# Performance work log

Hardware: AMD Instinct MI355X
Metric: run time of the kernel (lower is better)

Reference implementation:

```python
import jax, jax.numpy as jnp
import numpy as np

N, D_IN, D_K = 8192, 512, 64


def setup_inputs() -> dict:
    key = jax.random.key(0)
    k0, k1, k2, k3 = jax.random.split(key, 4)
    return {
        "inputs": jax.random.normal(k0, (N, D_IN), dtype=jnp.float32),
        "Wq": jax.random.normal(k1, (D_K, D_IN), dtype=jnp.float32),
        "Wk": jax.random.normal(k2, (D_K, D_IN), dtype=jnp.float32),
        "Wv": jax.random.normal(k3, (D_K, D_IN), dtype=jnp.float32),
    }


def reference(inputs, Wq, Wk, Wv):
    # nn.Linear(bias=False): x @ W.T, W has shape [out, in]
    q = inputs @ Wq.T  # [N, Dk]
    k = inputs @ Wk.T  # [N, Dk]
    v = inputs @ Wv.T  # [N, Dk]
    scaled = (q @ k.T) / jnp.sqrt(jnp.float32(D_K))  # [N, N]
    attn = jax.nn.softmax(scaled, axis=1)            # softmax over keys (dim=1)
    # weighted = values[:,None] * attn.T[:,:,None]; sum over dim 0 == attn @ v
    return attn @ v  # [N, Dk]
```

## Files before the change

kernel.cpp:

```cpp
#include <hip/hip_runtime.h>
#include <hip/hip_bf16.h>


#define N_TOK 8192
#define D_INN 512
#define DK    64

typedef __attribute__((ext_vector_type(8))) short bf16x8;
typedef __attribute__((ext_vector_type(4))) float f32x4;

static __device__ __forceinline__ unsigned f2bf_u(float f) {
  union { float f; unsigned u; } v; v.f = f;
  return (v.u + 0x7FFFu + ((v.u >> 16) & 1u)) >> 16;
}
static __device__ __forceinline__ unsigned short f2bf(float f) { return (unsigned short)f2bf_u(f); }
static __device__ __forceinline__ float bf2f(unsigned short h) {
  union { unsigned u; float f; } v; v.u = ((unsigned)h) << 16; return v.f;
}
static __device__ __forceinline__ unsigned truncpk(float a, float b) {
  union { float f; unsigned u; } x, y; x.f = a; y.f = b;
  return (x.u >> 16) | (y.u & 0xFFFF0000u);
}
static __device__ __forceinline__ void split2(float a, float b, unsigned& hi, unsigned& lo) {
  unsigned ha = f2bf_u(a), hb = f2bf_u(b);
  float ra = a - bf2f((unsigned short)ha);
  float rb = b - bf2f((unsigned short)hb);
  hi = ha | (hb << 16);
  lo = f2bf_u(ra) | (f2bf_u(rb) << 16);
}
static __device__ __forceinline__ void split8(const float* p, bf16x8& hi, bf16x8& lo) {
  float4 a = *(const float4*)p;
  float4 b = *(const float4*)(p + 4);
  union { unsigned u[4]; bf16x8 v; } H, L;
  split2(a.x, a.y, H.u[0], L.u[0]);
  split2(a.z, a.w, H.u[1], L.u[1]);
  split2(b.x, b.y, H.u[2], L.u[2]);
  split2(b.z, b.w, H.u[3], L.u[3]);
  hi = H.v; lo = L.v;
}
static __device__ __forceinline__ bf16x8 round8(const float* p) {
  float4 a = *(const float4*)p;
  float4 b = *(const float4*)(p + 4);
  union { unsigned u[4]; bf16x8 v; } H;
  H.u[0] = f2bf_u(a.x) | (f2bf_u(a.y) << 16);
  H.u[1] = f2bf_u(a.z) | (f2bf_u(a.w) << 16);
  H.u[2] = f2bf_u(b.x) | (f2bf_u(b.y) << 16);
  H.u[3] = f2bf_u(b.z) | (f2bf_u(b.w) << 16);
  return H.v;
}

__global__ __launch_bounds__(256, 2) void qkv3(
    const float* __restrict__ X,
    const float* __restrict__ Wq, const float* __restrict__ Wk, const float* __restrict__ Wv,
    unsigned short* __restrict__ qhp, unsigned short* __restrict__ qlp,
    unsigned short* __restrict__ kph, unsigned short* __restrict__ kpl,
    unsigned short* __restrict__ vp) {
  const int tid = threadIdx.x, w = tid >> 6, l = tid & 63;
  const int l15 = l & 15, g = l >> 4;
  const int t0 = blockIdx.x * 16;
  const int dq = w * 16;

  f32x4 aq = {0.f, 0.f, 0.f, 0.f}, ak = aq, av = aq;

  for (int kc = 0; kc < D_INN; kc += 32) {
    bf16x8 ah, al;
    split8(X + (t0 + l15) * D_INN + kc + g * 8, ah, al);

    const int woff = (dq + l15) * D_INN + kc + g * 8;
    bf16x8 bqh, bql, bkh, bkl;
    split8(Wq + woff, bqh, bql);
    split8(Wk + woff, bkh, bkl);
    bf16x8 bvh = round8(Wv + woff);

    aq = __builtin_amdgcn_mfma_f32_16x16x32_bf16(ah, bqh, aq, 0, 0, 0);
    aq = __builtin_amdgcn_mfma_f32_16x16x32_bf16(ah, bql, aq, 0, 0, 0);
    aq = __builtin_amdgcn_mfma_f32_16x16x32_bf16(al, bqh, aq, 0, 0, 0);
    ak = __builtin_amdgcn_mfma_f32_16x16x32_bf16(ah, bkh, ak, 0, 0, 0);
    ak = __builtin_amdgcn_mfma_f32_16x16x32_bf16(ah, bkl, ak, 0, 0, 0);
    ak = __builtin_amdgcn_mfma_f32_16x16x32_bf16(al, bkh, ak, 0, 0, 0);
    av = __builtin_amdgcn_mfma_f32_16x16x32_bf16(ah, bvh, av, 0, 0, 0);
    av = __builtin_amdgcn_mfma_f32_16x16x32_bf16(al, bvh, av, 0, 0, 0);
  }

#pragma unroll
  for (int r = 0; r < 4; r++) {
    float v = aq[r] * 0.125f;
    int row = t0 + g * 4 + r;
    unsigned short h = f2bf(v);
    qhp[row * DK + dq + l15] = h;
    qlp[row * DK + dq + l15] = f2bf(v - bf2f(h));
  }
#pragma unroll
  for (int r = 0; r < 4; r++) {
    float v = ak[r];
    int t = t0 + g * 4 + r;
    int d = dq + l15;
    int off = (t >> 5) * 2048 + ((t >> 4) & 1) * 1024 + (d >> 5) * 512 +
              ((t & 15) + (((d >> 3) & 3) << 4)) * 8 + (d & 7);
    unsigned short h = f2bf(v);
    kph[off] = h;
    kpl[off] = f2bf(v - bf2f(h));
  }
  {
    int tg = t0 + g * 4;
    int d = dq + l15;
    int off = (tg >> 5) * 2048 + (d >> 4) * 512 +
              (((d & 15) + (((tg >> 3) & 3) << 4))) * 8 + (tg & 7);
    uint2 pk;
    pk.x = f2bf_u(av[0]) | (f2bf_u(av[1]) << 16);
    pk.y = f2bf_u(av[2]) | (f2bf_u(av[3]) << 16);
    *(uint2*)(vp + off) = pk;
  }
}

__global__ __launch_bounds__(256, 2) void attn4(
    const unsigned short* __restrict__ qhp, const unsigned short* __restrict__ qlp,
    const unsigned short* __restrict__ kph, const unsigned short* __restrict__ kpl,
    const unsigned short* __restrict__ vp,
    unsigned short* __restrict__ pnb, float* __restrict__ pden, float* __restrict__ pM) {
  __shared__ unsigned short P_lds[4 * 2 * 16 * 72];

  const int tid = threadIdx.x, w = tid >> 6, l = tid & 63;
  const int l15 = l & 15, g = l >> 4;
  const int qblk = blockIdx.x >> 4, ks = blockIdx.x & 15;
  const int wq0 = qblk * 128 + w * 32;

  bf16x8 qhf[2][2], qlf[2][2];
#pragma unroll
  for (int u = 0; u < 2; u++)
#pragma unroll
    for (int c = 0; c < 2; c++) {
      int row = wq0 + u * 16 + l15;
      qhf[u][c] = *(const bf16x8*)(qhp + row * DK + c * 32 + g * 8);
      qlf[u][c] = *(const bf16x8*)(qlp + row * DK + c * 32 + g * 8);
    }

  const short onec = (short)0x3F80;
  const bf16x8 ones = {onec, onec, onec, onec, onec, onec, onec, onec};

  f32x4 accO[2][4], accL[2];
  float m[2] = {-1e30f, -1e30f};
#pragma unroll
  for (int u = 0; u < 2; u++) {
    accL[u] = f32x4{0.f, 0.f, 0.f, 0.f};
#pragma unroll
    for (int ds = 0; ds < 4; ds++) accO[u][ds] = f32x4{0.f, 0.f, 0.f, 0.f};
  }

  for (int kt = ks * 512; kt < ks * 512 + 512; kt += 64) {
    const int kti = kt >> 5;

    f32x4 st[2][4];
#pragma unroll
    for (int s = 0; s < 4; s++) {
      bf16x8 khf[2], klf[2];
#pragma unroll
      for (int c = 0; c < 2; c++) {
        const int off = (kti + (s >> 1)) * 2048 + (s & 1) * 1024 + c * 512 + l * 8;
        khf[c] = *(const bf16x8*)(kph + off);
        klf[c] = *(const bf16x8*)(kpl + off);
      }
      __builtin_amdgcn_s_setprio(1);
#pragma unroll
      for (int u = 0; u < 2; u++) {
        f32x4 sa = {0.f, 0.f, 0.f, 0.f};
        sa = __builtin_amdgcn_mfma_f32_16x16x32_bf16(khf[0], qhf[u][0], sa, 0, 0, 0);
        sa = __builtin_amdgcn_mfma_f32_16x16x32_bf16(khf[1], qhf[u][1], sa, 0, 0, 0);
        sa = __builtin_amdgcn_mfma_f32_16x16x32_bf16(khf[0], qlf[u][0], sa, 0, 0, 0);
        sa = __builtin_amdgcn_mfma_f32_16x16x32_bf16(khf[1], qlf[u][1], sa, 0, 0, 0);
        sa = __builtin_amdgcn_mfma_f32_16x16x32_bf16(klf[0], qhf[u][0], sa, 0, 0, 0);
        sa = __builtin_amdgcn_mfma_f32_16x16x32_bf16(klf[1], qhf[u][1], sa, 0, 0, 0);
        st[u][s] = sa;
      }
      __builtin_amdgcn_s_setprio(0);
    }

    bf16x8 vb[4][2];
#pragma unroll
    for (int ds = 0; ds < 4; ds++)
#pragma unroll
      for (int c = 0; c < 2; c++)
        vb[ds][c] = *(const bf16x8*)(vp + (kti + c) * 2048 + ds * 512 + l * 8);

    bf16x8 pa[2][2];
#pragma unroll
    for (int u = 0; u < 2; u++) {
      float t0m = fmaxf(fmaxf(st[u][0][0], st[u][0][1]), fmaxf(st[u][0][2], st[u][0][3]));
      float t1m = fmaxf(fmaxf(st[u][1][0], st[u][1][1]), fmaxf(st[u][1][2], st[u][1][3]));
      float t2m = fmaxf(fmaxf(st[u][2][0], st[u][2][1]), fmaxf(st[u][2][2], st[u][2][3]));
      float t3m = fmaxf(fmaxf(st[u][3][0], st[u][3][1]), fmaxf(st[u][3][2], st[u][3][3]));
      float tm = fmaxf(fmaxf(t0m, t1m), fmaxf(t2m, t3m));
      tm = fmaxf(tm, __shfl_xor(tm, 16, 64));
      tm = fmaxf(tm, __shfl_xor(tm, 32, 64));
      if (__any(tm > m[u] + 8.f)) {
        float mn = fmaxf(m[u], tm);
        float fac = __expf(m[u] - mn);
        m[u] = mn;
#pragma unroll
        for (int r = 0; r < 4; r++) {
          float fr = __shfl(fac, g * 4 + r, 64);
          accL[u][r] *= fr;
#pragma unroll
          for (int ds = 0; ds < 4; ds++) accO[u][ds][r] *= fr;
        }
      }
      const int base = ((w * 2 + u) * 16 + l15) * 72;
#pragma unroll
      for (int s = 0; s < 4; s++) {
        float p0 = __expf(st[u][s][0] - m[u]);
        float p1 = __expf(st[u][s][1] - m[u]);
        float p2 = __expf(st[u][s][2] - m[u]);
        float p3 = __expf(st[u][s][3] - m[u]);
        *(unsigned*)&P_lds[base + s * 16 + g * 4]     = truncpk(p0, p1);
        *(unsigned*)&P_lds[base + s * 16 + g * 4 + 2] = truncpk(p2, p3);
      }
#pragma unroll
      for (int c = 0; c < 2; c++)
        pa[u][c] = *(const bf16x8*)&P_lds[base + c * 32 + g * 8];
      accL[u] = __builtin_amdgcn_mfma_f32_16x16x32_bf16(pa[u][0], ones, accL[u], 0, 0, 0);
      accL[u] = __builtin_amdgcn_mfma_f32_16x16x32_bf16(pa[u][1], ones, accL[u], 0, 0, 0);
    }

    __builtin_amdgcn_s_setprio(1);
#pragma unroll
    for (int ds = 0; ds < 4; ds++)
#pragma unroll
      for (int u = 0; u < 2; u++) {
        accO[u][ds] = __builtin_amdgcn_mfma_f32_16x16x32_bf16(pa[u][0], vb[ds][0], accO[u][ds], 0, 0, 0);
        accO[u][ds] = __builtin_amdgcn_mfma_f32_16x16x32_bf16(pa[u][1], vb[ds][1], accO[u][ds], 0, 0, 0);
      }
    __builtin_amdgcn_s_setprio(0);
  }

#pragma unroll
  for (int u = 0; u < 2; u++) {
#pragma unroll
    for (int ds = 0; ds < 4; ds++)
#pragma unroll
      for (int r = 0; r < 4; r++)
        pnb[(size_t)ks * (N_TOK * DK) + (wq0 + u * 16 + g * 4 + r) * DK + ds * 16 + l15] =
            f2bf(accO[u][ds][r]);
    if (l15 == 0) {
#pragma unroll
      for (int r = 0; r < 4; r++) pden[ks * N_TOK + wq0 + u * 16 + g * 4 + r] = accL[u][r];
    }
    if (g == 0) pM[ks * N_TOK + wq0 + u * 16 + l15] = m[u];
  }
}

__global__ __launch_bounds__(256) void merge16(
    const unsigned short* __restrict__ pnb, const float* __restrict__ pden,
    const float* __restrict__ pM, float* __restrict__ out) {
  int i = blockIdx.x * 256 + threadIdx.x;
  int q = i >> 6, d = i & 63;
  float M = -1e30f;
#pragma unroll
  for (int s = 0; s < 16; s++) M = fmaxf(M, pM[s * N_TOK + q]);
  float num = 0.f, den = 0.f;
#pragma unroll
  for (int s = 0; s < 16; s++) {
    float e = __expf(pM[s * N_TOK + q] - M);
    num += bf2f(pnb[(size_t)s * (N_TOK * DK) + q * DK + d]) * e;
    den += pden[s * N_TOK + q] * e;
  }
  out[i] = num / den;
}

extern "C" void kernel_launch(void* const* d_in, const int* in_sizes, int n_in,
                              void* d_out, int out_size, void* d_ws, size_t ws_size,
                              hipStream_t stream) {
  (void)in_sizes; (void)n_in; (void)out_size; (void)ws_size;
  const float* X  = (const float*)d_in[0];
  const float* Wq = (const float*)d_in[1];
  const float* Wk = (const float*)d_in[2];
  const float* Wv = (const float*)d_in[3];

  char* base = (char*)d_ws;
  unsigned short* pnb = (unsigned short*)(base);
  unsigned short* qhp = (unsigned short*)(base + 16777216);
  unsigned short* qlp = (unsigned short*)(base + 17825792);
  unsigned short* kph = (unsigned short*)(base + 18874368);
  unsigned short* kpl = (unsigned short*)(base + 19922944);
  unsigned short* vp  = (unsigned short*)(base + 20971520);
  float* pden = (float*)(base + 22020096);
  float* pM   = (float*)(base + 22544384);

  qkv3<<<N_TOK / 16, 256, 0, stream>>>(X, Wq, Wk, Wv, qhp, qlp, kph, kpl, vp);
  attn4<<<1024, 256, 0, stream>>>(qhp, qlp, kph, kpl, vp, pnb, pden, pM);
  merge16<<<(N_TOK * DK) / 256, 256, 0, stream>>>(pnb, pden, pM, (float*)d_out);
}
```

Baseline: 148.0 us.

## Stage K/V tiles in LDS via double-buffered global_load_lds shared across waves

Each block now copies its K-hi, K-lo and V tiles into a double-buffered LDS area using direct global-to-LDS loads, prefetching the next tile while computing on the current one. The four waves then read K and V fragments from LDS instead of each fetching them from global memory, which removes redundant global/L2 traffic. The per-wave P scratch buffer is shrunk and reused across both row groups. This adds a block barrier per tile and raises LDS usage, which may limit occupancy. Correctness depends on the barrier also waiting for the asynchronous LDS loads to finish.

```diff
diff --git a/kernel.cpp b/kernel.cpp
--- a/kernel.cpp
+++ b/kernel.cpp
@@ -8,6 +8,11 @@
 
 typedef __attribute__((ext_vector_type(8))) short bf16x8;
 typedef __attribute__((ext_vector_type(4))) float f32x4;
+
+#define GLOAD_LDS16(gsrc, ldst) \
+  __builtin_amdgcn_global_load_lds( \
+      (const __attribute__((address_space(1))) unsigned int*)(gsrc), \
+      (__attribute__((address_space(3))) unsigned int*)(ldst), 16, 0, 0)
 
 static __device__ __forceinline__ unsigned f2bf_u(float f) {
   union { float f; unsigned u; } v; v.f = f;
@@ -113,12 +118,28 @@
   }
 }
 
-__global__ __launch_bounds__(256, 2) void attn4(
+static __device__ __forceinline__ void stage_tile(
+    const unsigned short* __restrict__ kph, const unsigned short* __restrict__ kpl,
+    const unsigned short* __restrict__ vp, int kti,
+    unsigned short* lds, int w, int l) {
+  const unsigned short* kb = kph + kti * 2048;
+  const unsigned short* lb = kpl + kti * 2048;
+  const unsigned short* vb = vp + kti * 2048;
+#pragma unroll
+  for (int j = 0; j < 6; ++j) {
+    int chunk = w * 6 + j;
+    const unsigned short* src = (chunk < 8) ? kb : ((chunk < 16) ? lb : vb);
+    GLOAD_LDS16(src + (chunk & 7) * 512 + l * 8, lds + chunk * 512);
+  }
+}
+
+__global__ __launch_bounds__(256, 2) void attn5(
     const unsigned short* __restrict__ qhp, const unsigned short* __restrict__ qlp,
     const unsigned short* __restrict__ kph, const unsigned short* __restrict__ kpl,
     const unsigned short* __restrict__ vp,
     unsigned short* __restrict__ pnb, float* __restrict__ pden, float* __restrict__ pM) {
-  __shared__ unsigned short P_lds[4 * 2 * 16 * 72];
+  __shared__ unsigned short kv_lds[2 * 12288];
+  __shared__ unsigned short P_lds[4 * 16 * 72];
 
   const int tid = threadIdx.x, w = tid >> 6, l = tid & 63;
   const int l15 = l & 15, g = l >> 4;
@@ -147,8 +168,19 @@
     for (int ds = 0; ds < 4; ds++) accO[u][ds] = f32x4{0.f, 0.f, 0.f, 0.f};
   }
 
-  for (int kt = ks * 512; kt < ks * 512 + 512; kt += 64) {
-    const int kti = kt >> 5;
+  const int kti0 = ks * 16;
+  stage_tile(kph, kpl, vp, kti0, kv_lds, w, l);
+  __syncthreads();
+
+  for (int t = 0; t < 8; ++t) {
+    const int cb = (t & 1) ? 12288 : 0;
+    const int pb = 12288 - cb;
+    const int ktin = (t < 7) ? (kti0 + 2 * t + 2) : (kti0 + 2 * t);
+    stage_tile(kph, kpl, vp, ktin, kv_lds + pb, w, l);
+
+    const unsigned short* Kh = kv_lds + cb;
+    const unsigned short* Kl = Kh + 4096;
+    const unsigned short* Vv = Kh + 8192;
 
     f32x4 st[2][4];
 #pragma unroll
@@ -156,9 +188,9 @@
       bf16x8 khf[2], klf[2];
 #pragma unroll
       for (int c = 0; c < 2; c++) {
-        const int off = (kti + (s >> 1)) * 2048 + (s & 1) * 1024 + c * 512 + l * 8;
-        khf[c] = *(const bf16x8*)(kph + off);
-        klf[c] = *(const bf16x8*)(kpl + off);
+        const int off = (s >> 1) * 2048 + (s & 1) * 1024 + c * 512 + l * 8;
+        khf[c] = *(const bf16x8*)(Kh + off);
+        klf[c] = *(const bf16x8*)(Kl + off);
       }
       __builtin_amdgcn_s_setprio(1);
 #pragma unroll
@@ -174,13 +206,6 @@
       }
       __builtin_amdgcn_s_setprio(0);
     }
-
-    bf16x8 vb[4][2];
-#pragma unroll
-    for (int ds = 0; ds < 4; ds++)
-#pragma unroll
-      for (int c = 0; c < 2; c++)
-        vb[ds][c] = *(const bf16x8*)(vp + (kti + c) * 2048 + ds * 512 + l * 8);
 
     bf16x8 pa[2][2];
 #pragma unroll
@@ -204,7 +229,7 @@
           for (int ds = 0; ds < 4; ds++) accO[u][ds][r] *= fr;
         }
       }
-      const int base = ((w * 2 + u) * 16 + l15) * 72;
+      const int base = (w * 16 + l15) * 72;
 #pragma unroll
       for (int s = 0; s < 4; s++) {
         float p0 = __expf(st[u][s][0] - m[u]);
@@ -223,13 +248,20 @@
 
     __builtin_amdgcn_s_setprio(1);
 #pragma unroll
-    for (int ds = 0; ds < 4; ds++)
+    for (int ds = 0; ds < 4; ds++) {
+      bf16x8 vb[2];
+#pragma unroll
+      for (int c = 0; c < 2; c++)
+        vb[c] = *(const bf16x8*)(Vv + c * 2048 + ds * 512 + l * 8);
 #pragma unroll
       for (int u = 0; u < 2; u++) {
-        accO[u][ds] = __builtin_amdgcn_mfma_f32_16x16x32_bf16(pa[u][0], vb[ds][0], accO[u][ds], 0, 0, 0);
-        accO[u][ds] = __builtin_amdgcn_mfma_f32_16x16x32_bf16(pa[u][1], vb[ds][1], accO[u][ds], 0, 0, 0);
-      }
+        accO[u][ds] = __builtin_amdgcn_mfma_f32_16x16x32_bf16(pa[u][0], vb[0], accO[u][ds], 0, 0, 0);
+        accO[u][ds] = __builtin_amdgcn_mfma_f32_16x16x32_bf16(pa[u][1], vb[1], accO[u][ds], 0, 0, 0);
+      }
+    }
     __builtin_amdgcn_s_setprio(0);
+
+    __syncthreads();
   }
 
 #pragma unroll
@@ -286,6 +318,6 @@
   float* pM   = (float*)(base + 22544384);
 
   qkv3<<<N_TOK / 16, 256, 0, stream>>>(X, Wq, Wk, Wv, qhp, qlp, kph, kpl, vp);
-  attn4<<<1024, 256, 0, stream>>>(qhp, qlp, kph, kpl, vp, pnb, pden, pM);
+  attn5<<<1024, 256, 0, stream>>>(qhp, qlp, kph, kpl, vp, pnb, pden, pM);
   merge16<<<(N_TOK * DK) / 256, 256, 0, stream>>>(pnb, pden, pM, (float*)d_out);
 }
```

Result: no change. 149.3 us (+0.8%).
